# Kernel tuning notes

Hardware: AMD Instinct MI355X
Metric: run time of the kernel (lower is better)

The kernel has to match this reference:

```python
import jax, jax.numpy as jnp
import numpy as np

FEATURES = 512
SPLIT_TT = 2
DK = FEATURES // SPLIT_TT           # 256: key width = features // split_tt
NUM_TAPE = 2048                     # ac_config.num_tape_tokens
THRESHOLD = 4.0                     # ac_config.dynamic_tape_length.act_epsilon
TOPK = int(NUM_TAPE // THRESHOLD)   # 512
TOKENS_PER_STEP = 16                # num_token_per_step
BATCH = 64


def setup_inputs() -> dict:
    key = jax.random.key(0)
    kq, kt = jax.random.split(key)
    return {
        "query": jax.random.normal(kq, (BATCH, DK), jnp.float32),
        "halting_prob": jnp.zeros((BATCH,), jnp.float32),
        "remainders": jnp.zeros((BATCH,), jnp.float32),
        "n_updates": jnp.zeros((BATCH,), jnp.float32),
        "score_mask": jnp.zeros((BATCH, NUM_TAPE), jnp.float32),
        "tape_tokens": jax.random.normal(kt, (BATCH, NUM_TAPE, FEATURES), jnp.float32),
    }


def reference(query, halting_prob, remainders, n_updates, score_mask, tape_tokens):
    # One ACT step (take_a_step / act_step) with bank_type='input',
    # act_loss_type='entropy', complex_query=True.
    still_running = (halting_prob < THRESHOLD).astype(jnp.float32)   # [B]

    # keys are the first DK features of the per-example tape bank
    keys = tape_tokens[:, :, :DK]                                    # [B, N, DK]
    scores = jnp.einsum('bd,bnd->bn', query, keys)                   # [B, N]

    # mask already-selected tokens, then top-k
    topk_idx = jax.lax.top_k(scores - score_mask * 1e9, TOPK)[1]     # [B, K] int32

    # NOTE: faithful to original: jnp.take without axis => FLAT gather into
    # scores.ravel(); indices in [0, N) all address row 0 of scores.
    weights = jnp.take(scores, topk_idx)                             # [B, K]
    weights = jax.nn.softmax(weights / (query.shape[-1] ** 0.5), axis=-1)

    entropy = 1.0 - jnp.sum(weights ** 2, axis=-1)                   # [B]
    sum_weights = jnp.sum(weights[:, :TOKENS_PER_STEP], axis=-1)     # [B]

    new_halted = (halting_prob + sum_weights >= THRESHOLD).astype(jnp.float32) * still_running
    still_running = still_running - new_halted
    remainders = remainders + (new_halted + still_running) * entropy
    halting_prob = halting_prob + sum_weights * still_running
    halting_prob = halting_prob + new_halted * (THRESHOLD - halting_prob)
    n_updates = n_updates + still_running + new_halted

    # gather selected tape tokens per example, softmax-weighted merge
    token_sel = jnp.take_along_axis(tape_tokens, topk_idx[..., None], axis=1)  # [B, K, F]
    token_sel = jnp.sum(token_sel * weights[..., None], axis=-2, keepdims=True)  # [B, 1, F]

    # scatter-accumulate selection mask
    score_mask = score_mask + jnp.sum(jax.nn.one_hot(topk_idx, NUM_TAPE), axis=1)  # [B, N]

    # complex_query update
    token_sel_keys = token_sel[:, :, :DK]                            # [B, 1, DK]
    query = (query + jnp.mean(token_sel_keys, axis=1)) / 2.0         # [B, DK]

    return (query, halting_prob, remainders, n_updates, score_mask, token_sel)
```

## Files before the change

### kernel.cpp

```cpp
#include <hip/hip_runtime.h>
#include <math.h>

#define BATCH 64
#define DK 256
#define FEATURES 512
#define NUM_TAPE 2048
#define TOPK 512
#define TOP16 16
#define THRESH 4.0f
#define KCHUNKS 4
#define KPER (TOPK / KCHUNKS)
#define CAP 640

#define OFF_Q 0
#define OFF_HP (BATCH * DK)
#define OFF_REM (OFF_HP + BATCH)
#define OFF_NUP (OFF_REM + BATCH)
#define OFF_MASK (OFF_NUP + BATCH)
#define OFF_TSEL (OFF_MASK + BATCH * NUM_TAPE)

#define WS_SCORES 0
#define WS_PART 131072

__device__ __forceinline__ unsigned f2key(float f) {
    unsigned u = __float_as_uint(f);
    return (u & 0x80000000u) ? ~u : (u | 0x80000000u);
}

#define RADIX_FIND(KREM)                                              \
    {                                                                 \
        int v = 0, hcnt = 0;                                          \
        if (tid < 256) {                                              \
            hcnt = hist[tid];                                         \
            hist[tid] = 0;                                            \
            v = hcnt;                                                 \
            _Pragma("unroll") for (int off = 1; off < 64; off <<= 1) {\
                const int t = __shfl_down(v, off);                    \
                if (lane + off < 64) v += t;                          \
            }                                                         \
            if (lane == 0) chunkTot[wv] = v;                          \
        }                                                             \
        __syncthreads();                                              \
        if (tid < 256) {                                              \
            _Pragma("unroll") for (int w2 = 0; w2 < 4; ++w2)          \
                if (w2 > wv) v += chunkTot[w2];                       \
            if (v >= (KREM) && (v - hcnt) < (KREM)) {                 \
                sh_digit = tid;                                       \
                sh_hi = v - hcnt;                                     \
            }                                                         \
        }                                                             \
        __syncthreads();                                              \
    }

__global__ __launch_bounds__(256) void k_scores(const float* __restrict__ q,
                                                const float* __restrict__ tape,
                                                float* __restrict__ scores) {
    const int b = blockIdx.y;
    const int tid = threadIdx.x;
    const int sub = tid & 7;
    const int tok = blockIdx.x * 32 + (tid >> 3);
    const float4* qp = reinterpret_cast<const float4*>(q + (size_t)b * DK);
    const float4* tp =
        reinterpret_cast<const float4*>(tape + ((size_t)b * NUM_TAPE + tok) * FEATURES);
    float s = 0.f;
#pragma unroll
    for (int j = 0; j < 8; ++j) {
        const float4 qf = qp[sub + 8 * j];
        const float4 tf = tp[sub + 8 * j];
        s += qf.x * tf.x + qf.y * tf.y + qf.z * tf.z + qf.w * tf.w;
    }
    s += __shfl_xor(s, 1);
    s += __shfl_xor(s, 2);
    s += __shfl_xor(s, 4);
    if (sub == 0) scores[b * NUM_TAPE + tok] = s;
}

__global__ __launch_bounds__(512) void k_select_gather(
    const float* __restrict__ scores, const float* __restrict__ mask_in,
    const float* __restrict__ hp_in, const float* __restrict__ rem_in,
    const float* __restrict__ nup_in, const float* __restrict__ tape,
    float* __restrict__ partials, float* __restrict__ out) {
    const int b = blockIdx.y;
    const int kc = blockIdx.x;
    const int tid = threadIdx.x;
    const int lane = tid & 63;
    const int wv = tid >> 6;

    __shared__ int hist[256];
    __shared__ int chunkTot[4];
    __shared__ int sh_digit, sh_hi;
    __shared__ unsigned ckey[CAP];
    __shared__ int cidx[CAP];
    __shared__ int csel[CAP];
    __shared__ int cand_n;
    __shared__ float redf[3][8];
    __shared__ int wtot[8];
    __shared__ float gl_w[KPER];
    __shared__ int gl_idx[KPER];
    __shared__ float4 shacc[512];

    const float4 sc = reinterpret_cast<const float4*>(scores + (size_t)b * NUM_TAPE)[tid];
    const float4 mk = reinterpret_cast<const float4*>(mask_in + (size_t)b * NUM_TAPE)[tid];
    const float4 s0 = reinterpret_cast<const float4*>(scores)[tid];
    unsigned key[4];
    key[0] = f2key(sc.x - mk.x * 1e9f);
    key[1] = f2key(sc.y - mk.y * 1e9f);
    key[2] = f2key(sc.z - mk.z * 1e9f);
    key[3] = f2key(sc.w - mk.w * 1e9f);
    const float s0v[4] = {s0.x * 0.0625f, s0.y * 0.0625f, s0.z * 0.0625f, s0.w * 0.0625f};

    if (tid < 256) hist[tid] = 0;
    __syncthreads();
#pragma unroll
    for (int j = 0; j < 4; ++j) atomicAdd(&hist[key[j] >> 24], 1);
    __syncthreads();
    RADIX_FIND(TOPK);
    const unsigned B1 = (unsigned)sh_digit;
    const int aboveA = sh_hi;
#pragma unroll
    for (int j = 0; j < 4; ++j)
        if ((key[j] >> 24) == B1) atomicAdd(&hist[(key[j] >> 16) & 0xFF], 1);
    __syncthreads();
    RADIX_FIND(TOPK - aboveA);
    const unsigned P16 = (B1 << 8) | (unsigned)sh_digit;
    const int krem512 = (TOPK - aboveA) - sh_hi;

    if (tid == 0) cand_n = 0;
    __syncthreads();
    int cpos[4];
#pragma unroll
    for (int j = 0; j < 4; ++j) {
        cpos[j] = -1;
        if ((key[j] >> 16) == P16) {
            const int p = atomicAdd(&cand_n, 1);
            if (p < CAP) {
                ckey[p] = key[j];
                cidx[p] = 4 * tid + j;
            }
            cpos[j] = p;
        }
    }
    __syncthreads();
    int cn = cand_n < CAP ? cand_n : CAP;
    for (int t = tid; t < cn; t += 512) {
        const unsigned k = ckey[t];
        const int i = cidx[t];
        int r = 0;
        for (int u = 0; u < cn; ++u) {
            const unsigned ko = ckey[u];
            r += (ko > k) || (ko == k && cidx[u] < i);
        }
        csel[t] = (r < krem512);
    }
    __syncthreads();
    bool sel[4];
#pragma unroll
    for (int j = 0; j < 4; ++j)
        sel[j] = ((key[j] >> 16) > P16) ||
                 (cpos[j] >= 0 && cpos[j] < CAP && csel[cpos[j]]);
    __syncthreads();

#pragma unroll
    for (int j = 0; j < 4; ++j)
        if (sel[j]) atomicAdd(&hist[key[j] >> 24], 1);
    __syncthreads();
    RADIX_FIND(TOP16);
    const unsigned C1 = (unsigned)sh_digit;
    const int aboveC = sh_hi;
#pragma unroll
    for (int j = 0; j < 4; ++j)
        if (sel[j] && (key[j] >> 24) == C1) atomicAdd(&hist[(key[j] >> 16) & 0xFF], 1);
    __syncthreads();
    RADIX_FIND(TOP16 - aboveC);
    const unsigned P16_2 = (C1 << 8) | (unsigned)sh_digit;
    const int krem16 = (TOP16 - aboveC) - sh_hi;

    if (tid == 0) cand_n = 0;
    __syncthreads();
    int c2pos[4];
#pragma unroll
    for (int j = 0; j < 4; ++j) {
        c2pos[j] = -1;
        if (sel[j] && (key[j] >> 16) == P16_2) {
            const int p = atomicAdd(&cand_n, 1);
            if (p < CAP) {
                ckey[p] = key[j];
                cidx[p] = 4 * tid + j;
            }
            c2pos[j] = p;
        }
    }
    __syncthreads();
    cn = cand_n < CAP ? cand_n : CAP;
    for (int t = tid; t < cn; t += 512) {
        const unsigned k = ckey[t];
        const int i = cidx[t];
        int r = 0;
        for (int u = 0; u < cn; ++u) {
            const unsigned ko = ckey[u];
            r += (ko > k) || (ko == k && cidx[u] < i);
        }
        csel[t] = (r < krem16);
    }
    __syncthreads();
    bool in16[4];
#pragma unroll
    for (int j = 0; j < 4; ++j)
        in16[j] = sel[j] && (((key[j] >> 16) > P16_2) ||
                             (c2pos[j] >= 0 && c2pos[j] < CAP && csel[c2pos[j]]));

    float ev[4];
    float se = 0.f, se2 = 0.f, s16l = 0.f;
#pragma unroll
    for (int j = 0; j < 4; ++j) {
        ev[j] = sel[j] ? expf(s0v[j]) : 0.f;
        se += ev[j];
        se2 += ev[j] * ev[j];
        if (in16[j]) s16l += ev[j];
    }
#pragma unroll
    for (int off = 32; off; off >>= 1) {
        se += __shfl_xor(se, off);
        se2 += __shfl_xor(se2, off);
        s16l += __shfl_xor(s16l, off);
    }
    if (lane == 0) {
        redf[0][wv] = se;
        redf[1][wv] = se2;
        redf[2][wv] = s16l;
    }
    __syncthreads();
    float S = 0.f, S2 = 0.f, S16 = 0.f;
#pragma unroll
    for (int w2 = 0; w2 < 8; ++w2) {
        S += redf[0][w2];
        S2 += redf[1][w2];
        S16 += redf[2][w2];
    }
    const float inv = 1.0f / S;
    const float sumsq = S2 * inv * inv;
    const float s16 = S16 * inv;

    float w[4];
#pragma unroll
    for (int j = 0; j < 4; ++j) w[j] = ev[j] * inv;

    {
        const int cnt = (sel[0] ? 1 : 0) + (sel[1] ? 1 : 0) + (sel[2] ? 1 : 0) + (sel[3] ? 1 : 0);
        int pre = cnt;
#pragma unroll
        for (int off = 1; off < 64; off <<= 1) {
            const int t = __shfl_up(pre, off);
            if (lane >= off) pre += t;
        }
        if (lane == 63) wtot[wv] = pre;
        __syncthreads();
        int base = 0;
        for (int w2 = 0; w2 < wv; ++w2) base += wtot[w2];
        int p = base + pre - cnt;
        const int lo = kc * KPER, hi = lo + KPER;
#pragma unroll
        for (int j = 0; j < 4; ++j) {
            if (sel[j]) {
                if (p >= lo && p < hi) {
                    gl_idx[p - lo] = 4 * tid + j;
                    gl_w[p - lo] = w[j];
                }
                ++p;
            }
        }
    }

    if (kc == 0) {
        if (tid == 0) {
            const float hp = hp_in[b], rem = rem_in[b], nup = nup_in[b];
            const float entropy = 1.0f - sumsq;
            const float still = (hp < THRESH) ? 1.f : 0.f;
            const float nh = ((hp + s16) >= THRESH ? 1.f : 0.f) * still;
            const float st2 = still - nh;
            out[OFF_REM + b] = rem + (nh + st2) * entropy;
            float hp1 = hp + s16 * st2;
            hp1 = hp1 + nh * (THRESH - hp1);
            out[OFF_HP + b] = hp1;
            out[OFF_NUP + b] = nup + st2 + nh;
        }
        float4 om;
        om.x = mk.x + (sel[0] ? 1.f : 0.f);
        om.y = mk.y + (sel[1] ? 1.f : 0.f);
        om.z = mk.z + (sel[2] ? 1.f : 0.f);
        om.w = mk.w + (sel[3] ? 1.f : 0.f);
        reinterpret_cast<float4*>(out + OFF_MASK + (size_t)b * NUM_TAPE)[tid] = om;
    }
    __syncthreads();

    const int rs = tid >> 7;
    const int f4 = tid & 127;
    float4 acc = {0.f, 0.f, 0.f, 0.f};
#pragma unroll 4
    for (int k = rs; k < KPER; k += 4) {
        const float ww = gl_w[k];
        const float4 t =
            reinterpret_cast<const float4*>(tape + ((size_t)b * NUM_TAPE + gl_idx[k]) * FEATURES)[f4];
        acc.x = fmaf(ww, t.x, acc.x);
        acc.y = fmaf(ww, t.y, acc.y);
        acc.z = fmaf(ww, t.z, acc.z);
        acc.w = fmaf(ww, t.w, acc.w);
    }
    shacc[tid] = acc;
    __syncthreads();
    if (tid < 128) {
        const float4 a0 = shacc[f4];
        const float4 a1 = shacc[128 + f4];
        const float4 a2 = shacc[256 + f4];
        const float4 a3 = shacc[384 + f4];
        float4 r;
        r.x = (a0.x + a1.x) + (a2.x + a3.x);
        r.y = (a0.y + a1.y) + (a2.y + a3.y);
        r.z = (a0.z + a1.z) + (a2.z + a3.z);
        r.w = (a0.w + a1.w) + (a2.w + a3.w);
        reinterpret_cast<float4*>(partials + ((size_t)b * KCHUNKS + kc) * FEATURES)[f4] = r;
    }
}

__global__ __launch_bounds__(128) void k_finish(const float* __restrict__ q,
                                                const float* __restrict__ partials,
                                                float* __restrict__ out) {
    const int b = blockIdx.x;
    const int f4 = threadIdx.x;
    const float4* pp = reinterpret_cast<const float4*>(partials + (size_t)b * KCHUNKS * FEATURES);
    const float4 a0 = pp[0 * 128 + f4];
    const float4 a1 = pp[1 * 128 + f4];
    const float4 a2 = pp[2 * 128 + f4];
    const float4 a3 = pp[3 * 128 + f4];
    float4 s;
    s.x = (a0.x + a1.x) + (a2.x + a3.x);
    s.y = (a0.y + a1.y) + (a2.y + a3.y);
    s.z = (a0.z + a1.z) + (a2.z + a3.z);
    s.w = (a0.w + a1.w) + (a2.w + a3.w);
    reinterpret_cast<float4*>(out + OFF_TSEL + (size_t)b * FEATURES)[f4] = s;
    if (f4 < 64) {
        const float4 qv = reinterpret_cast<const float4*>(q + (size_t)b * DK)[f4];
        float4 nq;
        nq.x = (qv.x + s.x) * 0.5f;
        nq.y = (qv.y + s.y) * 0.5f;
        nq.z = (qv.z + s.z) * 0.5f;
        nq.w = (qv.w + s.w) * 0.5f;
        reinterpret_cast<float4*>(out + OFF_Q + (size_t)b * DK)[f4] = nq;
    }
}

extern "C" void kernel_launch(void* const* d_in, const int* in_sizes, int n_in,
                              void* d_out, int out_size, void* d_ws, size_t ws_size,
                              hipStream_t stream) {
    const float* q = (const float*)d_in[0];
    const float* hp = (const float*)d_in[1];
    const float* rem = (const float*)d_in[2];
    const float* nup = (const float*)d_in[3];
    const float* mask = (const float*)d_in[4];
    const float* tape = (const float*)d_in[5];
    float* out = (float*)d_out;
    float* ws = (float*)d_ws;

    float* scores = ws + WS_SCORES;
    float* partials = ws + WS_PART;

    k_scores<<<dim3(NUM_TAPE / 32, BATCH), 256, 0, stream>>>(q, tape, scores);
    k_select_gather<<<dim3(KCHUNKS, BATCH), 512, 0, stream>>>(
        scores, mask, hp, rem, nup, tape, partials, out);
    k_finish<<<BATCH, 128, 0, stream>>>(q, partials, out);
}
```

Baseline: 45.00 us.

## Split top-k gather across 8 chunks and restructure per-block row accumulation

```diff
diff --git a/kernel.cpp b/kernel.cpp
--- a/kernel.cpp
+++ b/kernel.cpp
@@ -8,7 +8,7 @@
 #define TOPK 512
 #define TOP16 16
 #define THRESH 4.0f
-#define KCHUNKS 4
+#define KCHUNKS 8
 #define KPER (TOPK / KCHUNKS)
 #define CAP 640
 
@@ -97,7 +97,7 @@
     __shared__ int wtot[8];
     __shared__ float gl_w[KPER];
     __shared__ int gl_idx[KPER];
-    __shared__ float4 shacc[512];
+    __shared__ float4 shacc[1024];
 
     const float4 sc = reinterpret_cast<const float4*>(scores + (size_t)b * NUM_TAPE)[tid];
     const float4 mk = reinterpret_cast<const float4*>(mask_in + (size_t)b * NUM_TAPE)[tid];
@@ -120,13 +120,12 @@
 #pragma unroll
     for (int j = 0; j < 4; ++j)
         if ((key[j] >> 24) == B1) atomicAdd(&hist[(key[j] >> 16) & 0xFF], 1);
+    if (tid == 511) cand_n = 0;
     __syncthreads();
     RADIX_FIND(TOPK - aboveA);
     const unsigned P16 = (B1 << 8) | (unsigned)sh_digit;
     const int krem512 = (TOPK - aboveA) - sh_hi;
 
-    if (tid == 0) cand_n = 0;
-    __syncthreads();
     int cpos[4];
 #pragma unroll
     for (int j = 0; j < 4; ++j) {
@@ -170,13 +169,12 @@
 #pragma unroll
     for (int j = 0; j < 4; ++j)
         if (sel[j] && (key[j] >> 24) == C1) atomicAdd(&hist[(key[j] >> 16) & 0xFF], 1);
+    if (tid == 511) cand_n = 0;
     __syncthreads();
     RADIX_FIND(TOP16 - aboveC);
     const unsigned P16_2 = (C1 << 8) | (unsigned)sh_digit;
     const int krem16 = (TOP16 - aboveC) - sh_hi;
 
-    if (tid == 0) cand_n = 0;
-    __syncthreads();
     int c2pos[4];
 #pragma unroll
     for (int j = 0; j < 4; ++j) {
@@ -293,32 +291,40 @@
     }
     __syncthreads();
 
-    const int rs = tid >> 7;
-    const int f4 = tid & 127;
-    float4 acc = {0.f, 0.f, 0.f, 0.f};
-#pragma unroll 4
-    for (int k = rs; k < KPER; k += 4) {
+    const int rg = tid >> 6;
+    const int fl = tid & 63;
+    float4 acc0 = {0.f, 0.f, 0.f, 0.f};
+    float4 acc1 = {0.f, 0.f, 0.f, 0.f};
+#pragma unroll 2
+    for (int k = rg; k < KPER; k += 8) {
         const float ww = gl_w[k];
-        const float4 t =
-            reinterpret_cast<const float4*>(tape + ((size_t)b * NUM_TAPE + gl_idx[k]) * FEATURES)[f4];
-        acc.x = fmaf(ww, t.x, acc.x);
-        acc.y = fmaf(ww, t.y, acc.y);
-        acc.z = fmaf(ww, t.z, acc.z);
-        acc.w = fmaf(ww, t.w, acc.w);
-    }
-    shacc[tid] = acc;
+        const float4* rp =
+            reinterpret_cast<const float4*>(tape + ((size_t)b * NUM_TAPE + gl_idx[k]) * FEATURES);
+        const float4 t0 = rp[fl];
+        const float4 t1 = rp[64 + fl];
+        acc0.x = fmaf(ww, t0.x, acc0.x);
+        acc0.y = fmaf(ww, t0.y, acc0.y);
+        acc0.z = fmaf(ww, t0.z, acc0.z);
+        acc0.w = fmaf(ww, t0.w, acc0.w);
+        acc1.x = fmaf(ww, t1.x, acc1.x);
+        acc1.y = fmaf(ww, t1.y, acc1.y);
+        acc1.z = fmaf(ww, t1.z, acc1.z);
+        acc1.w = fmaf(ww, t1.w, acc1.w);
+    }
+    shacc[rg * 128 + fl] = acc0;
+    shacc[rg * 128 + 64 + fl] = acc1;
     __syncthreads();
     if (tid < 128) {
-        const float4 a0 = shacc[f4];
-        const float4 a1 = shacc[128 + f4];
-        const float4 a2 = shacc[256 + f4];
-        const float4 a3 = shacc[384 + f4];
-        float4 r;
-        r.x = (a0.x + a1.x) + (a2.x + a3.x);
-        r.y = (a0.y + a1.y) + (a2.y + a3.y);
-        r.z = (a0.z + a1.z) + (a2.z + a3.z);
-        r.w = (a0.w + a1.w) + (a2.w + a3.w);
-        reinterpret_cast<float4*>(partials + ((size_t)b * KCHUNKS + kc) * FEATURES)[f4] = r;
+        float4 s = {0.f, 0.f, 0.f, 0.f};
+#pragma unroll
+        for (int r = 0; r < 8; ++r) {
+            const float4 a = shacc[r * 128 + tid];
+            s.x += a.x;
+            s.y += a.y;
+            s.z += a.z;
+            s.w += a.w;
+        }
+        reinterpret_cast<float4*>(partials + ((size_t)b * KCHUNKS + kc) * FEATURES)[tid] = s;
     }
 }
 
@@ -328,15 +334,15 @@
     const int b = blockIdx.x;
     const int f4 = threadIdx.x;
     const float4* pp = reinterpret_cast<const float4*>(partials + (size_t)b * KCHUNKS * FEATURES);
-    const float4 a0 = pp[0 * 128 + f4];
-    const float4 a1 = pp[1 * 128 + f4];
-    const float4 a2 = pp[2 * 128 + f4];
-    const float4 a3 = pp[3 * 128 + f4];
-    float4 s;
-    s.x = (a0.x + a1.x) + (a2.x + a3.x);
-    s.y = (a0.y + a1.y) + (a2.y + a3.y);
-    s.z = (a0.z + a1.z) + (a2.z + a3.z);
-    s.w = (a0.w + a1.w) + (a2.w + a3.w);
+    float4 s = {0.f, 0.f, 0.f, 0.f};
+#pragma unroll
+    for (int r = 0; r < KCHUNKS; ++r) {
+        const float4 a = pp[r * 128 + f4];
+        s.x += a.x;
+        s.y += a.y;
+        s.z += a.z;
+        s.w += a.w;
+    }
     reinterpret_cast<float4*>(out + OFF_TSEL + (size_t)b * FEATURES)[f4] = s;
     if (f4 < 64) {
         const float4 qv = reinterpret_cast<const float4*>(q + (size_t)b * DK)[f4];
```

After: 46.40 us. 1.03x slower.
